# Optimization experiments

Measured on AMD Instinct MI355X. Metric: run time of the kernel, lower is better.

The kernel has to match this reference:

```python
import jax, jax.numpy as jnp
import numpy as np

N = 50000        # num nodes
NREL = 20        # base relations
R = 2 * NREL + 1 # relations incl. inverses + self-loop
NHID = 16
NCLASS = 50
E = 1_600_000    # base (directed) edges


def setup_inputs() -> dict:
    key = jax.random.key(0)
    k1, k2, k3, k4, k5 = jax.random.split(key, 5)
    src = jax.random.randint(k1, (E,), 0, N)
    rel = jax.random.randint(k2, (E,), 0, NREL)
    dst = jax.random.randint(k3, (E,), 0, N)
    W1 = jax.random.normal(k4, (R, N, NHID), jnp.float32) * 0.01   # featureless layer-1 weights
    b1 = jnp.zeros((NHID,), jnp.float32)
    W2 = jax.random.normal(k5, (R, NHID, NCLASS), jnp.float32) * 0.05
    b2 = jnp.zeros((NCLASS,), jnp.float32)
    return {"src": src, "rel": rel, "dst": dst, "W1": W1, "b1": b1, "W2": W2, "b2": b2}


def reference(src, rel, dst, W1, b1, W2, b2):
    nodes = jnp.arange(N)
    # augment with inverse relations and self-loop relation (id 2*NREL)
    s = jnp.concatenate([src, dst, nodes])
    o = jnp.concatenate([dst, src, nodes])
    r = jnp.concatenate([rel, rel + NREL, jnp.full((N,), 2 * NREL, dtype=rel.dtype)])

    # sum_sparse normalization: divide each edge value by its vertical-stacking row sum,
    # i.e. per-(relation, source) degree. Self-loops guarantee touched rows have deg >= 1.
    row_v = r * N + s                                   # vertical-stacked row index in [0, R*N)
    deg = jax.ops.segment_sum(jnp.ones(s.shape, jnp.float32), row_v, num_segments=R * N)
    vals = 1.0 / deg[row_v]                              # [E_total]

    # layer 1 (featureless, horizontal stacking): out[s] += val * W1[r, o]
    msg1 = vals[:, None] * W1.reshape(R * N, NHID)[r * N + o]        # [E_total, NHID]
    h = jax.ops.segment_sum(msg1, s, num_segments=N) + b1            # [N, NHID]
    h = jax.nn.relu(h)                                                # dropout p=0.0 -> identity

    # layer 2 (vertical stacking): AF[r*N+s] += val * h[o], then contract with W2
    msg2 = vals[:, None] * h[o]                                       # [E_total, NHID]
    af = jax.ops.segment_sum(msg2, row_v, num_segments=R * N).reshape(R, N, NHID)
    logits = jnp.einsum('rnh,rho->no', af, W2) + b2                   # [N, NCLASS]
    return jax.nn.log_softmax(logits, axis=1)
```

## Files before the change

kernel.cpp:

```cpp
#include <hip/hip_runtime.h>

#define NN     50000
#define NRELB  20
#define RR     (2*NRELB + 1)
#define NHID   16
#define NCLASS 50
#define EB     1600000
#define RH     (RR * NHID)
#define STRIDE 128
#define KPAD   672
#define KU32   (KPAD/2)
#define NKB    21
#define NCT    4
#define NROWS  50048
#define PM     72
#define AGW    4

#define NBIN   391
#define BINCAP 12288
#define TILE   2048
#define EPT    8

using f16x8 = __attribute__((ext_vector_type(8))) _Float16;
using f32x4 = __attribute__((ext_vector_type(4))) float;
using u16x8 = __attribute__((ext_vector_type(8))) unsigned short;

__global__ __launch_bounds__(256) void scat1_kernel(
        const int* __restrict__ src, const int* __restrict__ rel,
        const int* __restrict__ dst,
        unsigned* __restrict__ gBinCur, unsigned* __restrict__ gRecs) {
    __shared__ unsigned binCnt[NBIN], binOff[NBIN], binBase[NBIN];
    const int tid = threadIdx.x;
    for (int i = tid; i < NBIN; i += 256) { binCnt[i] = 0u; binOff[i] = 0u; }
    __syncthreads();

    const int e0 = blockIdx.x * TILE;
    unsigned rec[2 * EPT], bn[2 * EPT];
    bool val[EPT];
    #pragma unroll
    for (int k = 0; k < EPT; ++k) {
        int e = e0 + k * 256 + tid;
        val[k] = (e < EB);
        unsigned s = 0, r = 0, o = 0;
        if (val[k]) { s = (unsigned)src[e]; r = (unsigned)rel[e]; o = (unsigned)dst[e]; }
        bn[2*k]    = s >> 7;
        rec[2*k]   = ((s & 127u) << 22) | (r << 16) | o;
        bn[2*k+1]  = o >> 7;
        rec[2*k+1] = ((o & 127u) << 22) | ((r + NRELB) << 16) | s;
    }
    #pragma unroll
    for (int k = 0; k < EPT; ++k)
        if (val[k]) {
            atomicAdd(&binCnt[bn[2*k]], 1u);
            atomicAdd(&binCnt[bn[2*k+1]], 1u);
        }
    __syncthreads();
    for (int b = tid; b < NBIN; b += 256) {
        unsigned c = binCnt[b];
        if (c) binBase[b] = atomicAdd(&gBinCur[b], c);
    }
    __syncthreads();
    #pragma unroll
    for (int k = 0; k < 2 * EPT; ++k)
        if (val[k >> 1]) {
            unsigned b = bn[k];
            unsigned pos = binBase[b] + atomicAdd(&binOff[b], 1u);
            if (pos < BINCAP) gRecs[(size_t)b * BINCAP + pos] = rec[k];
        }
}

__global__ __launch_bounds__(256) void scat2_kernel(
        const unsigned* __restrict__ gBinCur, const unsigned* __restrict__ gRecs,
        unsigned* __restrict__ cnt, unsigned* __restrict__ ekey) {
    __shared__ unsigned off[128];
    const int b = blockIdx.x, tid = threadIdx.x;
    if (tid < 128) off[tid] = 1u;
    __syncthreads();
    const unsigned M = min(gBinCur[b], (unsigned)BINCAP);
    const unsigned* recs = gRecs + (size_t)b * BINCAP;
    for (unsigned i0 = 0; i0 < M; i0 += 1024) {
        unsigned i;
        unsigned r0 = 0, r1 = 0, r2 = 0, r3 = 0;
        bool v0, v1, v2, v3;
        i = i0 + tid;        v0 = i < M; if (v0) r0 = recs[i];
        i = i0 + 256 + tid;  v1 = i < M; if (v1) r1 = recs[i];
        i = i0 + 512 + tid;  v2 = i < M; if (v2) r2 = recs[i];
        i = i0 + 768 + tid;  v3 = i < M; if (v3) r3 = recs[i];
        if (v0) {
            unsigned sl = r0 >> 22, slot = atomicAdd(&off[sl], 1u), n = b * 128u + sl;
            if (slot < STRIDE && n < NN) ekey[(size_t)n * STRIDE + slot] = r0 & 0x3FFFFFu;
        }
        if (v1) {
            unsigned sl = r1 >> 22, slot = atomicAdd(&off[sl], 1u), n = b * 128u + sl;
            if (slot < STRIDE && n < NN) ekey[(size_t)n * STRIDE + slot] = r1 & 0x3FFFFFu;
        }
        if (v2) {
            unsigned sl = r2 >> 22, slot = atomicAdd(&off[sl], 1u), n = b * 128u + sl;
            if (slot < STRIDE && n < NN) ekey[(size_t)n * STRIDE + slot] = r2 & 0x3FFFFFu;
        }
        if (v3) {
            unsigned sl = r3 >> 22, slot = atomicAdd(&off[sl], 1u), n = b * 128u + sl;
            if (slot < STRIDE && n < NN) ekey[(size_t)n * STRIDE + slot] = r3 & 0x3FFFFFu;
        }
    }
    __syncthreads();
    if (tid < 128) {
        unsigned n = b * 128u + (unsigned)tid;
        if (n < NN) {
            ekey[(size_t)n * STRIDE] = ((unsigned)(2 * NRELB) << 16) | n;
            cnt[n] = min(off[tid], (unsigned)STRIDE);
        }
    }
}

__device__ __forceinline__ void mk_afrags(u16x8 rv, int m,
                                          f16x8& a0, f16x8& a1, f16x8& a2) {
    #pragma unroll
    for (int j = 0; j < 8; ++j) {
        a0[j] = (_Float16)(rv[j] == (unsigned short)m);
        a1[j] = (_Float16)(rv[j] == (unsigned short)(m + 16));
        a2[j] = (_Float16)(rv[j] == (unsigned short)(m + 32));
    }
}

__global__ __launch_bounds__(256) void layer1_kernel(
        const unsigned* __restrict__ ekey, const unsigned* __restrict__ cnt,
        const float* __restrict__ W1, const float* __restrict__ b1,
        float* __restrict__ h) {
    __shared__ __align__(16) _Float16 rT[AGW][16 * PM];
    __shared__ __align__(16) unsigned short relc[AGW][64];
    __shared__ float degL[AGW][48];
    const int wave = threadIdx.x >> 6, lane = threadIdx.x & 63;
    const int n = blockIdx.x * AGW + wave;
    const unsigned* ek = ekey + (size_t)n * STRIDE;
    const int deg = cnt[n];
    const int m = lane & 15;

    if (lane < 48) degL[wave][lane] = 0.f;
    {
        unsigned* rz = (unsigned*)&rT[wave][0];
        #pragma unroll
        for (int t = 0; t < 9; ++t) rz[lane + t * 64] = 0u;
    }

    f32x4 d0 = {0.f, 0.f, 0.f, 0.f};
    f32x4 d1 = {0.f, 0.f, 0.f, 0.f};
    f32x4 d2 = {0.f, 0.f, 0.f, 0.f};

    for (int c0 = 0; c0 < deg; c0 += 64) {
        const int degc = min(deg - c0, 64);
        {
            int r = 63;
            if (lane < degc) r = (int)(ek[c0 + lane] >> 16);
            relc[wave][lane] = (unsigned short)r;
            if (lane < degc) atomicAdd(&degL[wave][r], 1.f);
        }
        {
            const int g = lane >> 2, q = (lane & 3) * 4;
            for (int i = 0; i < degc; i += 16) {
                int kl = min(i + g, degc - 1);
                unsigned key = ek[c0 + kl];
                int r = key >> 16, o = key & 0xFFFF;
                float4 v = *(const float4*)(W1 + ((size_t)(r * NN + o)) * NHID + q);
                rT[wave][(q + 0) * PM + kl] = (_Float16)v.x;
                rT[wave][(q + 1) * PM + kl] = (_Float16)v.y;
                rT[wave][(q + 2) * PM + kl] = (_Float16)v.z;
                rT[wave][(q + 3) * PM + kl] = (_Float16)v.w;
            }
        }
        const int nkt = (degc > 32) ? 2 : 1;
        for (int kt = 0; kt < nkt; ++kt) {
            const int ko = kt * 32 + (lane >> 4) * 8;
            f16x8 b = *(const f16x8*)&rT[wave][m * PM + ko];
            u16x8 rv = *(const u16x8*)&relc[wave][ko];
            f16x8 a0, a1, a2;
            mk_afrags(rv, m, a0, a1, a2);
            d0 = __builtin_amdgcn_mfma_f32_16x16x32_f16(a0, b, d0, 0, 0, 0);
            d1 = __builtin_amdgcn_mfma_f32_16x16x32_f16(a1, b, d1, 0, 0, 0);
            d2 = __builtin_amdgcn_mfma_f32_16x16x32_f16(a2, b, d2, 0, 0, 0);
        }
    }

    float partial = 0.f;
    const int rg = lane >> 4;
    #pragma unroll
    for (int mt = 0; mt < 3; ++mt) {
        f32x4 dv = (mt == 0) ? d0 : (mt == 1) ? d1 : d2;
        #pragma unroll
        for (int c = 0; c < 4; ++c) {
            int r = mt * 16 + rg * 4 + c;
            if (r < RR) {
                float dgc = degL[wave][r];
                partial += (dgc != 0.f) ? dv[c] / dgc : 0.f;
            }
        }
    }
    partial += __shfl_xor(partial, 16);
    partial += __shfl_xor(partial, 32);
    if (lane < NHID) h[n * NHID + lane] = fmaxf(partial + b1[lane], 0.f);
}

__global__ __launch_bounds__(256) void agg_kernel(
        const unsigned* __restrict__ ekey, const unsigned* __restrict__ cnt,
        const float* __restrict__ h, unsigned* __restrict__ af) {
    __shared__ __align__(16) _Float16 rT[AGW][16 * PM];
    __shared__ __align__(16) unsigned short relc[AGW][64];
    __shared__ float degL[AGW][48];
    const int wave = threadIdx.x >> 6, lane = threadIdx.x & 63;
    const int n = blockIdx.x * AGW + wave;
    const unsigned* ek = ekey + (size_t)n * STRIDE;
    const int deg = cnt[n];
    const int m = lane & 15;

    if (lane < 48) degL[wave][lane] = 0.f;
    {
        unsigned* rz = (unsigned*)&rT[wave][0];
        #pragma unroll
        for (int t = 0; t < 9; ++t) rz[lane + t * 64] = 0u;
    }

    f32x4 d0 = {0.f, 0.f, 0.f, 0.f};
    f32x4 d1 = {0.f, 0.f, 0.f, 0.f};
    f32x4 d2 = {0.f, 0.f, 0.f, 0.f};

    for (int c0 = 0; c0 < deg; c0 += 64) {
        const int degc = min(deg - c0, 64);
        {
            int r = 63;
            if (lane < degc) r = (int)(ek[c0 + lane] >> 16);
            relc[wave][lane] = (unsigned short)r;
            if (lane < degc) atomicAdd(&degL[wave][r], 1.f);
        }
        {
            const int g = lane >> 2, q = (lane & 3) * 4;
            for (int i = 0; i < degc; i += 16) {
                int kl = min(i + g, degc - 1);
                unsigned key = ek[c0 + kl];
                float4 v = *(const float4*)(h + (key & 0xFFFF) * NHID + q);
                rT[wave][(q + 0) * PM + kl] = (_Float16)v.x;
                rT[wave][(q + 1) * PM + kl] = (_Float16)v.y;
                rT[wave][(q + 2) * PM + kl] = (_Float16)v.z;
                rT[wave][(q + 3) * PM + kl] = (_Float16)v.w;
            }
        }
        const int nkt = (degc > 32) ? 2 : 1;
        for (int kt = 0; kt < nkt; ++kt) {
            const int ko = kt * 32 + (lane >> 4) * 8;
            f16x8 b = *(const f16x8*)&rT[wave][m * PM + ko];
            u16x8 rv = *(const u16x8*)&relc[wave][ko];
            f16x8 a0, a1, a2;
            mk_afrags(rv, m, a0, a1, a2);
            d0 = __builtin_amdgcn_mfma_f32_16x16x32_f16(a0, b, d0, 0, 0, 0);
            d1 = __builtin_amdgcn_mfma_f32_16x16x32_f16(a1, b, d1, 0, 0, 0);
            d2 = __builtin_amdgcn_mfma_f32_16x16x32_f16(a2, b, d2, 0, 0, 0);
        }
    }

    _Float16* arow = (_Float16*)af + (size_t)n * KPAD;
    const int hh = lane & 15, rg = lane >> 4;
    #pragma unroll
    for (int mt = 0; mt < 3; ++mt) {
        f32x4 dv = (mt == 0) ? d0 : (mt == 1) ? d1 : d2;
        #pragma unroll
        for (int c = 0; c < 4; ++c) {
            int r = mt * 16 + rg * 4 + c;
            if (r <= RR) {
                float val = 0.f;
                if (r < RR) {
                    float dgc = degL[wave][r];
                    val = (dgc != 0.f) ? dv[c] / dgc : 0.f;
                }
                arow[r * 16 + hh] = (_Float16)val;
            }
        }
    }
}

__global__ void pack_kernel(const float* __restrict__ W2, _Float16* __restrict__ W2f) {
    int idx = blockIdx.x * blockDim.x + threadIdx.x;
    if (idx >= NCT * NKB * 64 * 8) return;
    int j = idx & 7, lane = (idx >> 3) & 63, t = idx >> 9;
    int kb = t % NKB, ct = t / NKB;
    int k = kb * 32 + (lane >> 4) * 8 + j;
    int c = ct * 16 + (lane & 15);
    W2f[idx] = (_Float16)((k < RH && c < NCLASS) ? W2[k * NCLASS + c] : 0.f);
}

__global__ __launch_bounds__(256) void gemm_kernel(
        const _Float16* __restrict__ af, const _Float16* __restrict__ W2f,
        const float* __restrict__ b2, float* __restrict__ out) {
    __shared__ float lg[4][16][68];
    const int wave = threadIdx.x >> 6, lane = threadIdx.x & 63;
    const int n0 = (blockIdx.x * 4 + wave) * 16;
    const int l15 = lane & 15, g = lane >> 4;

    f32x4 acc0 = {0.f,0.f,0.f,0.f}, acc1 = {0.f,0.f,0.f,0.f};
    f32x4 acc2 = {0.f,0.f,0.f,0.f}, acc3 = {0.f,0.f,0.f,0.f};

    const _Float16* arow = af + (size_t)(n0 + l15) * KPAD + g * 8;
    const _Float16* wrow = W2f + (size_t)lane * 8;
    for (int kb = 0; kb < NKB; ++kb) {
        f16x8 a = *(const f16x8*)(arow + kb * 32);
        f16x8 b0 = *(const f16x8*)(wrow + (size_t)(0 * NKB + kb) * 512);
        f16x8 b1 = *(const f16x8*)(wrow + (size_t)(1 * NKB + kb) * 512);
        f16x8 b2f = *(const f16x8*)(wrow + (size_t)(2 * NKB + kb) * 512);
        f16x8 b3 = *(const f16x8*)(wrow + (size_t)(3 * NKB + kb) * 512);
        acc0 = __builtin_amdgcn_mfma_f32_16x16x32_f16(a, b0, acc0, 0, 0, 0);
        acc1 = __builtin_amdgcn_mfma_f32_16x16x32_f16(a, b1, acc1, 0, 0, 0);
        acc2 = __builtin_amdgcn_mfma_f32_16x16x32_f16(a, b2f, acc2, 0, 0, 0);
        acc3 = __builtin_amdgcn_mfma_f32_16x16x32_f16(a, b3, acc3, 0, 0, 0);
    }

    #pragma unroll
    for (int ct = 0; ct < 4; ++ct) {
        f32x4 av = (ct == 0) ? acc0 : (ct == 1) ? acc1 : (ct == 2) ? acc2 : acc3;
        int c = ct * 16 + l15;
        float bias = (c < NCLASS) ? b2[c] : 0.f;
        #pragma unroll
        for (int reg = 0; reg < 4; ++reg)
            lg[wave][g * 4 + reg][c] = av[reg] + bias;
    }
    __syncthreads();

    for (int r = 0; r < 16; ++r) {
        const int n = n0 + r;
        float x = (lane < NCLASS) ? lg[wave][r][lane] : -INFINITY;
        float m = x;
        #pragma unroll
        for (int off = 32; off; off >>= 1) m = fmaxf(m, __shfl_xor(m, off));
        float ex = (lane < NCLASS) ? expf(x - m) : 0.f;
        float ss = ex;
        #pragma unroll
        for (int off = 32; off; off >>= 1) ss += __shfl_xor(ss, off);
        float ls = logf(ss) + m;
        if (lane < NCLASS && n < NN) out[n * NCLASS + lane] = x - ls;
    }
}

extern "C" void kernel_launch(void* const* d_in, const int* in_sizes, int n_in,
                              void* d_out, int out_size, void* d_ws, size_t ws_size,
                              hipStream_t stream) {
    const int*   src = (const int*)d_in[0];
    const int*   rel = (const int*)d_in[1];
    const int*   dst = (const int*)d_in[2];
    const float* W1  = (const float*)d_in[3];
    const float* b1  = (const float*)d_in[4];
    const float* W2  = (const float*)d_in[5];
    const float* b2  = (const float*)d_in[6];
    float* out = (float*)d_out;

    unsigned* cnt  = (unsigned*)d_ws;
    unsigned* ekey = cnt + NN;
    float*    h    = (float*)(ekey + (size_t)NN * STRIDE);
    unsigned* af   = (unsigned*)(h + (size_t)NN * NHID);
    _Float16* W2f  = (_Float16*)(af + (size_t)NROWS * KU32);
    unsigned* gBinCur = (unsigned*)(W2f + NCT * NKB * 512);
    unsigned* gRecs   = af;

    const int blk = 256;
    hipMemsetAsync(gBinCur, 0, 512 * sizeof(unsigned), stream);
    scat1_kernel<<<(EB + TILE - 1) / TILE, blk, 0, stream>>>(src, rel, dst, gBinCur, gRecs);
    scat2_kernel<<<NBIN, blk, 0, stream>>>(gBinCur, gRecs, cnt, ekey);
    pack_kernel<<<(NCT * NKB * 512 + blk - 1) / blk, blk, 0, stream>>>(W2, W2f);
    layer1_kernel<<<NN / AGW, blk, 0, stream>>>(ekey, cnt, W1, b1, h);
    agg_kernel<<<NN / AGW, blk, 0, stream>>>(ekey, cnt, h, af);
    gemm_kernel<<<NROWS / 64, blk, 0, stream>>>((const _Float16*)af, W2f, b2, out);
}
```

Baseline: 231.8 us.

## Fuse layer-2 aggregation with W2 GEMM and log-softmax via shared memory

Merges the agg and gemm kernels into one kernel. Each block aggregates 16 nodes (4 per wave, processed serially), keeps the fp16 AF rows in LDS, then each wave computes one 16-column tile of the W2 product and finishes with log-softmax. This removes the global AF buffer write and read-back plus one launch. In exchange, each wave handles four nodes sequentially, which may reduce latency hiding. The larger LDS footprint may lower occupancy, and gRecs now occupies a separate workspace region.

```diff
diff --git a/kernel.cpp b/kernel.cpp
--- a/kernel.cpp
+++ b/kernel.cpp
@@ -9,12 +9,13 @@
 #define RH     (RR * NHID)
 #define STRIDE 128
 #define KPAD   672
-#define KU32   (KPAD/2)
+#define APAD   680
 #define NKB    21
 #define NCT    4
 #define NROWS  50048
 #define PM     72
 #define AGW    4
+#define FNPB   16
 
 #define NBIN   391
 #define BINCAP 12288
@@ -143,9 +144,7 @@
         for (int t = 0; t < 9; ++t) rz[lane + t * 64] = 0u;
     }
 
-    f32x4 d0 = {0.f, 0.f, 0.f, 0.f};
-    f32x4 d1 = {0.f, 0.f, 0.f, 0.f};
-    f32x4 d2 = {0.f, 0.f, 0.f, 0.f};
+    f32x4 d0 = {0.f,0.f,0.f,0.f}, d1 = {0.f,0.f,0.f,0.f}, d2 = {0.f,0.f,0.f,0.f};
 
     for (int c0 = 0; c0 < deg; c0 += 64) {
         const int degc = min(deg - c0, 64);
@@ -200,82 +199,6 @@
     if (lane < NHID) h[n * NHID + lane] = fmaxf(partial + b1[lane], 0.f);
 }
 
-__global__ __launch_bounds__(256) void agg_kernel(
-        const unsigned* __restrict__ ekey, const unsigned* __restrict__ cnt,
-        const float* __restrict__ h, unsigned* __restrict__ af) {
-    __shared__ __align__(16) _Float16 rT[AGW][16 * PM];
-    __shared__ __align__(16) unsigned short relc[AGW][64];
-    __shared__ float degL[AGW][48];
-    const int wave = threadIdx.x >> 6, lane = threadIdx.x & 63;
-    const int n = blockIdx.x * AGW + wave;
-    const unsigned* ek = ekey + (size_t)n * STRIDE;
-    const int deg = cnt[n];
-    const int m = lane & 15;
-
-    if (lane < 48) degL[wave][lane] = 0.f;
-    {
-        unsigned* rz = (unsigned*)&rT[wave][0];
-        #pragma unroll
-        for (int t = 0; t < 9; ++t) rz[lane + t * 64] = 0u;
-    }
-
-    f32x4 d0 = {0.f, 0.f, 0.f, 0.f};
-    f32x4 d1 = {0.f, 0.f, 0.f, 0.f};
-    f32x4 d2 = {0.f, 0.f, 0.f, 0.f};
-
-    for (int c0 = 0; c0 < deg; c0 += 64) {
-        const int degc = min(deg - c0, 64);
-        {
-            int r = 63;
-            if (lane < degc) r = (int)(ek[c0 + lane] >> 16);
-            relc[wave][lane] = (unsigned short)r;
-            if (lane < degc) atomicAdd(&degL[wave][r], 1.f);
-        }
-        {
-            const int g = lane >> 2, q = (lane & 3) * 4;
-            for (int i = 0; i < degc; i += 16) {
-                int kl = min(i + g, degc - 1);
-                unsigned key = ek[c0 + kl];
-                float4 v = *(const float4*)(h + (key & 0xFFFF) * NHID + q);
-                rT[wave][(q + 0) * PM + kl] = (_Float16)v.x;
-                rT[wave][(q + 1) * PM + kl] = (_Float16)v.y;
-                rT[wave][(q + 2) * PM + kl] = (_Float16)v.z;
-                rT[wave][(q + 3) * PM + kl] = (_Float16)v.w;
-            }
-        }
-        const int nkt = (degc > 32) ? 2 : 1;
-        for (int kt = 0; kt < nkt; ++kt) {
-            const int ko = kt * 32 + (lane >> 4) * 8;
-            f16x8 b = *(const f16x8*)&rT[wave][m * PM + ko];
-            u16x8 rv = *(const u16x8*)&relc[wave][ko];
-            f16x8 a0, a1, a2;
-            mk_afrags(rv, m, a0, a1, a2);
-            d0 = __builtin_amdgcn_mfma_f32_16x16x32_f16(a0, b, d0, 0, 0, 0);
-            d1 = __builtin_amdgcn_mfma_f32_16x16x32_f16(a1, b, d1, 0, 0, 0);
-            d2 = __builtin_amdgcn_mfma_f32_16x16x32_f16(a2, b, d2, 0, 0, 0);
-        }
-    }
-
-    _Float16* arow = (_Float16*)af + (size_t)n * KPAD;
-    const int hh = lane & 15, rg = lane >> 4;
-    #pragma unroll
-    for (int mt = 0; mt < 3; ++mt) {
-        f32x4 dv = (mt == 0) ? d0 : (mt == 1) ? d1 : d2;
-        #pragma unroll
-        for (int c = 0; c < 4; ++c) {
-            int r = mt * 16 + rg * 4 + c;
-            if (r <= RR) {
-                float val = 0.f;
-                if (r < RR) {
-                    float dgc = degL[wave][r];
-                    val = (dgc != 0.f) ? dv[c] / dgc : 0.f;
-                }
-                arow[r * 16 + hh] = (_Float16)val;
-            }
-        }
-    }
-}
-
 __global__ void pack_kernel(const float* __restrict__ W2, _Float16* __restrict__ W2f) {
     int idx = blockIdx.x * blockDim.x + threadIdx.x;
     if (idx >= NCT * NKB * 64 * 8) return;
@@ -286,53 +209,116 @@
     W2f[idx] = (_Float16)((k < RH && c < NCLASS) ? W2[k * NCLASS + c] : 0.f);
 }
 
-__global__ __launch_bounds__(256) void gemm_kernel(
-        const _Float16* __restrict__ af, const _Float16* __restrict__ W2f,
+__global__ __launch_bounds__(256) void agg_gemm_kernel(
+        const unsigned* __restrict__ ekey, const unsigned* __restrict__ cnt,
+        const float* __restrict__ h, const _Float16* __restrict__ W2f,
         const float* __restrict__ b2, float* __restrict__ out) {
-    __shared__ float lg[4][16][68];
+    __shared__ __align__(16) _Float16 rT[4][16 * PM];
+    __shared__ __align__(16) unsigned short relc[4][64];
+    __shared__ float degL[4][48];
+    __shared__ __align__(16) _Float16 afL[FNPB][APAD];
+    __shared__ float lg[FNPB][68];
     const int wave = threadIdx.x >> 6, lane = threadIdx.x & 63;
-    const int n0 = (blockIdx.x * 4 + wave) * 16;
-    const int l15 = lane & 15, g = lane >> 4;
-
-    f32x4 acc0 = {0.f,0.f,0.f,0.f}, acc1 = {0.f,0.f,0.f,0.f};
-    f32x4 acc2 = {0.f,0.f,0.f,0.f}, acc3 = {0.f,0.f,0.f,0.f};
-
-    const _Float16* arow = af + (size_t)(n0 + l15) * KPAD + g * 8;
-    const _Float16* wrow = W2f + (size_t)lane * 8;
-    for (int kb = 0; kb < NKB; ++kb) {
-        f16x8 a = *(const f16x8*)(arow + kb * 32);
-        f16x8 b0 = *(const f16x8*)(wrow + (size_t)(0 * NKB + kb) * 512);
-        f16x8 b1 = *(const f16x8*)(wrow + (size_t)(1 * NKB + kb) * 512);
-        f16x8 b2f = *(const f16x8*)(wrow + (size_t)(2 * NKB + kb) * 512);
-        f16x8 b3 = *(const f16x8*)(wrow + (size_t)(3 * NKB + kb) * 512);
-        acc0 = __builtin_amdgcn_mfma_f32_16x16x32_f16(a, b0, acc0, 0, 0, 0);
-        acc1 = __builtin_amdgcn_mfma_f32_16x16x32_f16(a, b1, acc1, 0, 0, 0);
-        acc2 = __builtin_amdgcn_mfma_f32_16x16x32_f16(a, b2f, acc2, 0, 0, 0);
-        acc3 = __builtin_amdgcn_mfma_f32_16x16x32_f16(a, b3, acc3, 0, 0, 0);
-    }
-
-    #pragma unroll
-    for (int ct = 0; ct < 4; ++ct) {
-        f32x4 av = (ct == 0) ? acc0 : (ct == 1) ? acc1 : (ct == 2) ? acc2 : acc3;
-        int c = ct * 16 + l15;
+    const int nbase = blockIdx.x * FNPB;
+    const int m = lane & 15, g = lane >> 4;
+
+    {
+        unsigned* rz = (unsigned*)&rT[wave][0];
+        #pragma unroll
+        for (int t = 0; t < 9; ++t) rz[lane + t * 64] = 0u;
+    }
+
+    for (int nd = 0; nd < 4; ++nd) {
+        const int widx = wave * 4 + nd;
+        const int n = nbase + widx;
+        const unsigned* ek = ekey + (size_t)n * STRIDE;
+        const int deg = (n < NN) ? (int)cnt[n] : 0;
+
+        if (lane < 48) degL[wave][lane] = 0.f;
+
+        f32x4 d0 = {0.f,0.f,0.f,0.f}, d1 = {0.f,0.f,0.f,0.f}, d2 = {0.f,0.f,0.f,0.f};
+
+        for (int c0 = 0; c0 < deg; c0 += 64) {
+            const int degc = min(deg - c0, 64);
+            {
+                int r = 63;
+                if (lane < degc) r = (int)(ek[c0 + lane] >> 16);
+                relc[wave][lane] = (unsigned short)r;
+                if (lane < degc) atomicAdd(&degL[wave][r], 1.f);
+            }
+            {
+                const int gg = lane >> 2, q = (lane & 3) * 4;
+                for (int i = 0; i < degc; i += 16) {
+                    int kl = min(i + gg, degc - 1);
+                    unsigned key = ek[c0 + kl];
+                    float4 v = *(const float4*)(h + (key & 0xFFFF) * NHID + q);
+                    rT[wave][(q + 0) * PM + kl] = (_Float16)v.x;
+                    rT[wave][(q + 1) * PM + kl] = (_Float16)v.y;
+                    rT[wave][(q + 2) * PM + kl] = (_Float16)v.z;
+                    rT[wave][(q + 3) * PM + kl] = (_Float16)v.w;
+                }
+            }
+            const int nkt = (degc > 32) ? 2 : 1;
+            for (int kt = 0; kt < nkt; ++kt) {
+                const int ko = kt * 32 + g * 8;
+                f16x8 b = *(const f16x8*)&rT[wave][m * PM + ko];
+                u16x8 rv = *(const u16x8*)&relc[wave][ko];
+                f16x8 a0, a1, a2;
+                mk_afrags(rv, m, a0, a1, a2);
+                d0 = __builtin_amdgcn_mfma_f32_16x16x32_f16(a0, b, d0, 0, 0, 0);
+                d1 = __builtin_amdgcn_mfma_f32_16x16x32_f16(a1, b, d1, 0, 0, 0);
+                d2 = __builtin_amdgcn_mfma_f32_16x16x32_f16(a2, b, d2, 0, 0, 0);
+            }
+        }
+
+        const int hh = lane & 15, rg = lane >> 4;
+        #pragma unroll
+        for (int mt = 0; mt < 3; ++mt) {
+            f32x4 dv = (mt == 0) ? d0 : (mt == 1) ? d1 : d2;
+            #pragma unroll
+            for (int c = 0; c < 4; ++c) {
+                int r = mt * 16 + rg * 4 + c;
+                if (r <= RR) {
+                    float val = 0.f;
+                    if (r < RR) {
+                        float dgc = degL[wave][r];
+                        val = (dgc != 0.f) ? dv[c] / dgc : 0.f;
+                    }
+                    afL[widx][r * 16 + hh] = (_Float16)val;
+                }
+            }
+        }
+    }
+    __syncthreads();
+
+    {
+        f32x4 acc = {0.f, 0.f, 0.f, 0.f};
+        const _Float16* wrow = W2f + (size_t)lane * 8;
+        for (int kb = 0; kb < NKB; ++kb) {
+            f16x8 a = *(const f16x8*)&afL[m][kb * 32 + g * 8];
+            f16x8 b = *(const f16x8*)(wrow + (size_t)(wave * NKB + kb) * 512);
+            acc = __builtin_amdgcn_mfma_f32_16x16x32_f16(a, b, acc, 0, 0, 0);
+        }
+        int c = wave * 16 + m;
         float bias = (c < NCLASS) ? b2[c] : 0.f;
         #pragma unroll
         for (int reg = 0; reg < 4; ++reg)
-            lg[wave][g * 4 + reg][c] = av[reg] + bias;
-    }
-    __syncthreads();
-
-    for (int r = 0; r < 16; ++r) {
-        const int n = n0 + r;
-        float x = (lane < NCLASS) ? lg[wave][r][lane] : -INFINITY;
-        float m = x;
-        #pragma unroll
-        for (int off = 32; off; off >>= 1) m = fmaxf(m, __shfl_xor(m, off));
-        float ex = (lane < NCLASS) ? expf(x - m) : 0.f;
+            lg[g * 4 + reg][c] = acc[reg] + bias;
+    }
+    __syncthreads();
+
+    for (int rr = 0; rr < 4; ++rr) {
+        const int row = wave * 4 + rr;
+        const int n = nbase + row;
+        float x = (lane < NCLASS) ? lg[row][lane] : -INFINITY;
+        float mx = x;
+        #pragma unroll
+        for (int off = 32; off; off >>= 1) mx = fmaxf(mx, __shfl_xor(mx, off));
+        float ex = (lane < NCLASS) ? expf(x - mx) : 0.f;
         float ss = ex;
         #pragma unroll
         for (int off = 32; off; off >>= 1) ss += __shfl_xor(ss, off);
-        float ls = logf(ss) + m;
+        float ls = logf(ss) + mx;
         if (lane < NCLASS && n < NN) out[n * NCLASS + lane] = x - ls;
     }
 }
@@ -352,10 +338,9 @@
     unsigned* cnt  = (unsigned*)d_ws;
     unsigned* ekey = cnt + NN;
     float*    h    = (float*)(ekey + (size_t)NN * STRIDE);
-    unsigned* af   = (unsigned*)(h + (size_t)NN * NHID);
-    _Float16* W2f  = (_Float16*)(af + (size_t)NROWS * KU32);
+    _Float16* W2f  = (_Float16*)(h + (size_t)NN * NHID);
     unsigned* gBinCur = (unsigned*)(W2f + NCT * NKB * 512);
-    unsigned* gRecs   = af;
+    unsigned* gRecs   = gBinCur + 512;
 
     const int blk = 256;
     hipMemsetAsync(gBinCur, 0, 512 * sizeof(unsigned), stream);
@@ -363,6 +348,5 @@
     scat2_kernel<<<NBIN, blk, 0, stream>>>(gBinCur, gRecs, cnt, ekey);
     pack_kernel<<<(NCT * NKB * 512 + blk - 1) / blk, blk, 0, stream>>>(W2, W2f);
     layer1_kernel<<<NN / AGW, blk, 0, stream>>>(ekey, cnt, W1, b1, h);
-    agg_kernel<<<NN / AGW, blk, 0, stream>>>(ekey, cnt, h, af);
-    gemm_kernel<<<NROWS / 64, blk, 0, stream>>>((const _Float16*)af, W2f, b2, out);
-}
+    agg_gemm_kernel<<<NROWS / FNPB, blk, 0, stream>>>(ekey, cnt, h, W2f, b2, out);
+}
```

After: 232.6 us. No clear change (+0.3%).
